# Kernel optimization log

Hardware: AMD Instinct MI355X
Metric: run time of the kernel (lower is better)

The kernel has to match this reference:

```python
import jax, jax.numpy as jnp
import numpy as np

B, H, W, C, HEADS = 32, 56, 56, 384, 12
WIN = (7, 7)
SHIFT = (3, 3)
N = WIN[0] * WIN[1]
HD = C // HEADS
HIDDEN = int(C * 2.0)
CPB_HIDDEN = 512


def _cpb_tables():
    # log-spaced continuous relative coordinates table (SwinV2 CPB)
    coords = [np.arange(-(w - 1), w, dtype=np.float32) for w in WIN]
    g = np.stack(np.meshgrid(*coords, indexing='ij'))
    for i, w in enumerate(WIN):
        g[i] = g[i] / (w - 1)
    rel = np.moveaxis(g, 0, -1)[None]              # (1, 2w0-1, 2w1-1, 2)
    rel = 8.0 * rel
    rel = np.sign(rel) * np.log2(np.abs(rel) + 1.0) / np.log2(8.0)
    grid = np.stack(np.meshgrid(*[np.arange(w) for w in WIN], indexing='ij')).reshape(2, -1)
    dists = grid[:, :, None] - grid[:, None, :]    # (2, N, N)
    dists[0] = (dists[0] + WIN[0] - 1) * (2 * WIN[1] - 1)
    dists[1] = (dists[1] + WIN[1] - 1)
    return jnp.asarray(rel, jnp.float32), jnp.asarray(dists.sum(0), jnp.int32)

REL_TAB, RPB_IDX = _cpb_tables()


def _compute_mask():
    img = np.zeros((1, H, W, 1), np.float32)
    cnt = 0
    for s0 in (slice(0, -WIN[0]), slice(-WIN[0], -SHIFT[0]), slice(-SHIFT[0], None)):
        for s1 in (slice(0, -WIN[1]), slice(-WIN[1], -SHIFT[1]), slice(-SHIFT[1], None)):
            img[:, s0, s1, :] = cnt
            cnt += 1
    w = img.reshape(1, H // WIN[0], WIN[0], W // WIN[1], WIN[1], 1)
    w = w.transpose(0, 1, 3, 2, 4, 5).reshape(-1, N)
    m = w[:, None, :] - w[:, :, None]
    return jnp.asarray(np.where(m != 0, -100.0, 0.0).astype(np.float32))


def _layernorm(x, g, b, eps=1e-5):
    mu = x.mean(-1, keepdims=True)
    var = ((x - mu) ** 2).mean(-1, keepdims=True)
    return (x - mu) / jnp.sqrt(var + eps) * g + b


def _window_partition(x):
    b = x.shape[0]
    x = x.reshape(b, H // WIN[0], WIN[0], W // WIN[1], WIN[1], C)
    return x.transpose(0, 1, 3, 2, 4, 5).reshape(-1, N, C)


def _window_reverse(win):
    x = win.reshape(B, H // WIN[0], W // WIN[1], WIN[0], WIN[1], C)
    return x.transpose(0, 1, 3, 2, 4, 5).reshape(B, H, W, C)


def setup_inputs() -> dict:
    key = jax.random.key(0)
    ks = jax.random.split(key, 16)
    s = 0.02
    return {
        'x': jax.random.normal(ks[0], (B, H, W, C), jnp.float32),
        'attn_mask': _compute_mask(),                              # (nW, N, N)
        'norm1_g': jnp.ones((C,), jnp.float32),
        'norm1_b': jnp.zeros((C,), jnp.float32),
        'qkv_w': jax.random.normal(ks[1], (3 * C, C), jnp.float32) * s,
        'qkv_b': jnp.zeros((3 * C,), jnp.float32),
        'proj_w': jax.random.normal(ks[2], (C, C), jnp.float32) * s,
        'proj_b': jnp.zeros((C,), jnp.float32),
        'cpb_w1': jax.random.normal(ks[3], (CPB_HIDDEN, 2), jnp.float32) * s,
        'cpb_b1': jnp.zeros((CPB_HIDDEN,), jnp.float32),
        'cpb_w2': jax.random.normal(ks[4], (HEADS, CPB_HIDDEN), jnp.float32) * s,
        'logit_scale': jnp.full((HEADS, 1, 1), np.log(10.0), jnp.float32),
        'norm2_g': jnp.ones((C,), jnp.float32),
        'norm2_b': jnp.zeros((C,), jnp.float32),
        'mlp_w1': jax.random.normal(ks[5], (HIDDEN, C), jnp.float32) * s,
        'mlp_b1': jnp.zeros((HIDDEN,), jnp.float32),
        'mlp_w2': jax.random.normal(ks[6], (C, HIDDEN), jnp.float32) * s,
        'mlp_b2': jnp.zeros((C,), jnp.float32),
    }


def reference(x, attn_mask, norm1_g, norm1_b, qkv_w, qkv_b, proj_w, proj_b,
              cpb_w1, cpb_b1, cpb_w2, logit_scale, norm2_g, norm2_b,
              mlp_w1, mlp_b1, mlp_w2, mlp_b2):
    # continuous position bias: MLP over log-spaced rel coords, gathered per pair
    h = jax.nn.relu(REL_TAB @ cpb_w1.T + cpb_b1)       # (1, 2w0-1, 2w1-1, 512)
    tab = (h @ cpb_w2.T).reshape(-1, HEADS)            # ((2w0-1)*(2w1-1), heads)
    rpb = tab[RPB_IDX.reshape(-1)].reshape(N, N, HEADS)
    rpb = 16.0 * jax.nn.sigmoid(rpb)
    rpb = rpb.transpose(2, 0, 1)                       # (heads, N, N)

    shortcut = x
    xn = _layernorm(x, norm1_g, norm1_b)
    xs = jnp.roll(xn, (-SHIFT[0], -SHIFT[1]), axis=(1, 2))
    wnd = _window_partition(xs)                        # (B*nW, N, C)
    qkv = (wnd @ qkv_w.T + qkv_b).reshape(-1, N, 3, HEADS, HD)
    q = qkv[:, :, 0].transpose(0, 2, 1, 3)             # (B*nW, heads, N, hd)
    k = qkv[:, :, 1].transpose(0, 2, 1, 3)
    v = qkv[:, :, 2].transpose(0, 2, 1, 3)
    qn = q / jnp.maximum(jnp.linalg.norm(q, axis=-1, keepdims=True), 1e-12)
    kn = k / jnp.maximum(jnp.linalg.norm(k, axis=-1, keepdims=True), 1e-12)
    scale = jnp.exp(jnp.minimum(logit_scale, jnp.log(100.0)))   # (heads,1,1)
    attn = jnp.einsum('bhnd,bhmd->bhnm', qn, kn) * scale + rpb
    nW = attn_mask.shape[0]
    attn = attn.reshape(B, nW, HEADS, N, N) + attn_mask[None, :, None]
    attn = jax.nn.softmax(attn.reshape(-1, HEADS, N, N), axis=-1)
    o = jnp.einsum('bhnm,bhmd->bhnd', attn, v)
    o = o.transpose(0, 2, 1, 3).reshape(-1, N, C)
    o = o @ proj_w.T + proj_b
    xr = _window_reverse(o)
    xr = jnp.roll(xr, (SHIFT[0], SHIFT[1]), axis=(1, 2))
    x = shortcut + xr
    xm = _layernorm(x, norm2_g, norm2_b)
    xm = jax.nn.gelu(xm @ mlp_w1.T + mlp_b1, approximate=False) @ mlp_w2.T + mlp_b2
    return x + xm
```

## Files before the change

### kernel.cpp

```cpp
#include <hip/hip_runtime.h>
#include <stdint.h>

typedef unsigned short u16;
typedef __bf16 bf16x8 __attribute__((ext_vector_type(8)));
typedef float f32x4 __attribute__((ext_vector_type(4)));

__device__ __forceinline__ float b2f(u16 u) {
    union { float f; uint32_t i; } x; x.i = ((uint32_t)u) << 16; return x.f;
}
__device__ __forceinline__ u16 f2b(float f) {
    union { float f; uint32_t i; } x; x.f = f;
    uint32_t r = (x.i + 0x7fffu + ((x.i >> 16) & 1u)) >> 16;
    return (u16)r;
}
__device__ __forceinline__ void gll16(const void* g, void* l) {
    __builtin_amdgcn_global_load_lds((const __attribute__((address_space(1))) void*)g,
                                     (__attribute__((address_space(3))) void*)l, 16, 0, 0);
}

__global__ __launch_bounds__(512)
void cpb_tab_kernel(const float* __restrict__ w1, const float* __restrict__ b1,
                    const float* __restrict__ w2, float* __restrict__ tab) {
    __shared__ float hbuf[512];
    int p = blockIdx.x, j = threadIdx.x;
    int i0 = p / 13, i1 = p % 13;
    float c0 = (i0 - 6) * (8.0f / 6.0f), c1 = (i1 - 6) * (8.0f / 6.0f);
    float r0 = copysignf(log2f(fabsf(c0) + 1.0f) * (1.0f / 3.0f), c0);
    float r1 = copysignf(log2f(fabsf(c1) + 1.0f) * (1.0f / 3.0f), c1);
    float h = r0 * w1[j * 2] + r1 * w1[j * 2 + 1] + b1[j];
    hbuf[j] = fmaxf(h, 0.0f);
    __syncthreads();
    if (j < 12) {
        float s = 0.0f;
        for (int t = 0; t < 512; t++) s += w2[j * 512 + t] * hbuf[t];
        tab[p * 12 + j] = s;
    }
}

__global__ __launch_bounds__(256)
void cpb_gather_kernel(const float* __restrict__ tab, float* __restrict__ rpb) {
    int idx = blockIdx.x * 256 + threadIdx.x;
    if (idx >= 12 * 2401) return;
    int h = idx / 2401, r = idx % 2401, i = r / 49, j = r % 49;
    int d = (i / 7 - j / 7 + 6) * 13 + (i % 7 - j % 7 + 6);
    float v = tab[d * 12 + h];
    rpb[idx] = 16.0f / (1.0f + expf(-v));
}

__global__ __launch_bounds__(256)
void wconv_kernel(const float* __restrict__ s0, const float* __restrict__ s1,
                  const float* __restrict__ s2, const float* __restrict__ s3,
                  u16* __restrict__ dst) {
    int i = (blockIdx.x * 256 + threadIdx.x) * 4;
    if (i >= 1179648) return;
    const float* src; int off;
    if (i < 442368)      { src = s0; off = i; }
    else if (i < 589824) { src = s1; off = i - 442368; }
    else if (i < 884736) { src = s2; off = i - 589824; }
    else                 { src = s3; off = i - 884736; }
    float4 v = *(const float4*)(src + off);
    u16 o[4] = {f2b(v.x), f2b(v.y), f2b(v.z), f2b(v.w)};
    *(uint2*)(dst + i) = *(const uint2*)o;
}

template <int PERM>
__global__ __launch_bounds__(256)
void ln_fused_kernel(const float* __restrict__ in, const float* __restrict__ g,
                     const float* __restrict__ b, u16* __restrict__ outb) {
    int wave = threadIdx.x >> 6, lane = threadIdx.x & 63;
    int tok = blockIdx.x * 4 + wave;
    size_t src = (size_t)tok * 384;
    float2 v[3];
    float s = 0.0f, s2 = 0.0f;
#pragma unroll
    for (int i = 0; i < 3; i++) {
        v[i] = *(const float2*)&in[src + i * 128 + lane * 2];
        s += v[i].x + v[i].y;
        s2 += v[i].x * v[i].x + v[i].y * v[i].y;
    }
#pragma unroll
    for (int m = 32; m >= 1; m >>= 1) { s += __shfl_xor(s, m, 64); s2 += __shfl_xor(s2, m, 64); }
    float mu = s * (1.0f / 384.0f);
    float rstd = rsqrtf(s2 * (1.0f / 384.0f) - mu * mu + 1e-5f);
    int drow = tok;
    if (PERM) {
        int bb = tok / 3136, rr = tok % 3136;
        int h = rr / 56, w = rr % 56;
        int hs = h - 3; if (hs < 0) hs += 56;
        int wsr = w - 3; if (wsr < 0) wsr += 56;
        int wi = (hs / 7) * 8 + (wsr / 7);
        int n = (hs % 7) * 7 + (wsr % 7);
        drow = (bb * 64 + wi) * 49 + n;
    }
    size_t dst = (size_t)drow * 384;
#pragma unroll
    for (int i = 0; i < 3; i++) {
        int c = i * 128 + lane * 2;
        float2 gg = *(const float2*)&g[c];
        float2 bv = *(const float2*)&b[c];
        u16 o[2] = { f2b((v[i].x - mu) * rstd * gg.x + bv.x),
                     f2b((v[i].y - mu) * rstd * gg.y + bv.y) };
        *(uint32_t*)&outb[dst + c] = *(const uint32_t*)o;
    }
}

enum { SRC_PLAIN = 0, SRC_HEADMAJ = 1 };
enum { EPI_QKV = 0, EPI_PROJ = 1, EPI_MLP1 = 2, EPI_MLP2 = 3 };

template <int SRC, int EPI, int GX>
__global__ __launch_bounds__(256)
void gemm_mfma(const u16* __restrict__ A, const u16* __restrict__ Wb,
               const float* __restrict__ bias, int K,
               u16* __restrict__ o0, u16* __restrict__ o1, u16* __restrict__ o2,
               const float* __restrict__ xres, float* __restrict__ dout) {
    const int tid = threadIdx.x;
    const int wave = tid >> 6, lane = tid & 63, quad = lane >> 4, l16 = lane & 15;
    const int wm = (wave >> 1) * 64, wn = (wave & 1) * 64;
    const int bid = blockIdx.x;
    const int nb = (bid & 7) * ((int)gridDim.x >> 3) + (bid >> 3);
    const int m0 = (nb / GX) * 128, n0 = (nb % GX) * 128;
    __shared__ alignas(16) u16 lA[128 * 32];
    __shared__ alignas(16) u16 lB[128 * 32];
    f32x4 acc[4][4] = {};

    const int c4 = lane & 3, rsub = lane >> 2;
    size_t agb[2], wgb[2];
#pragma unroll
    for (int s = 0; s < 2; s++) {
        int row = (wave * 2 + s) * 16 + rsub;
        int swz = (c4 ^ ((row >> 1) & 3)) * 16;
        int grow = m0 + row;
        if (SRC == SRC_HEADMAJ) {
            int widx = grow / 49, n = grow % 49;
            agb[s] = ((size_t)widx * 18816 + (size_t)n * 32) * 2 + swz;
        } else {
            agb[s] = (size_t)grow * (size_t)K * 2 + swz;
        }
        wgb[s] = (size_t)(n0 + row) * (size_t)K * 2 + swz;
    }
    const char* Ac = (const char*)A;
    const char* Wc = (const char*)Wb;
    char* ldsA = (char*)lA;
    char* ldsB = (char*)lB;
    const int swzR = (quad ^ ((l16 >> 1) & 3)) * 16;

    for (int kk = 0; kk < K; kk += 32) {
        __syncthreads();
        size_t ka = (SRC == SRC_HEADMAJ) ? (size_t)(kk >> 5) * 3136 : (size_t)kk * 2;
        size_t kb = (size_t)kk * 2;
#pragma unroll
        for (int s = 0; s < 2; s++)
            gll16(Ac + agb[s] + ka, ldsA + (wave * 2 + s) * 1024);
#pragma unroll
        for (int s = 0; s < 2; s++)
            gll16(Wc + wgb[s] + kb, ldsB + (wave * 2 + s) * 1024);
        __syncthreads();
        bf16x8 af[4], bfr[4];
#pragma unroll
        for (int t = 0; t < 4; t++)
            af[t] = *(const bf16x8*)(ldsA + (wm + t * 16 + l16) * 64 + swzR);
#pragma unroll
        for (int t = 0; t < 4; t++)
            bfr[t] = *(const bf16x8*)(ldsB + (wn + t * 16 + l16) * 64 + swzR);
#pragma unroll
        for (int i = 0; i < 4; i++)
#pragma unroll
            for (int j = 0; j < 4; j++)
                acc[i][j] = __builtin_amdgcn_mfma_f32_16x16x32_bf16(af[i], bfr[j], acc[i][j], 0, 0, 0);
    }

#pragma unroll
    for (int i = 0; i < 4; i++) {
#pragma unroll
        for (int r = 0; r < 4; r++) {
            int row = m0 + wm + i * 16 + quad * 4 + r;
            int widx = 0, n = 0;
            size_t pbase = 0;
            if (EPI == EPI_QKV || EPI == EPI_PROJ) { widx = row / 49; n = row % 49; }
            if (EPI == EPI_PROJ) {
                int bb = widx >> 6, wi = widx & 63;
                int hs = (wi >> 3) * 7 + n / 7, wsr = (wi & 7) * 7 + n % 7;
                int h = hs + 3; if (h >= 56) h -= 56;
                int w = wsr + 3; if (w >= 56) w -= 56;
                pbase = (((size_t)bb * 56 + h) * 56 + w) * 384;
            }
#pragma unroll
            for (int j = 0; j < 4; j++) {
                int col = n0 + wn + j * 16 + l16;
                float v = acc[i][j][r] + bias[col];
                if (EPI == EPI_QKV) {
                    int which = col / 384, head = (col >> 5) % 12, hd = col & 31;
                    u16* dst = (which == 0) ? o0 : ((which == 1) ? o1 : o2);
                    dst[(size_t)(widx * 12 + head) * 1568 + n * 32 + hd] = f2b(v);
                } else if (EPI == EPI_PROJ) {
                    dout[pbase + col] = v + xres[pbase + col];
                } else if (EPI == EPI_MLP1) {
                    float ge = 0.5f * v * (1.0f + erff(v * 0.70710678f));
                    o0[(size_t)row * 768 + col] = f2b(ge);
                } else {
                    size_t o = (size_t)row * 384 + col;
                    dout[o] = v + dout[o];
                }
            }
        }
    }
}

__global__ __launch_bounds__(256)
void attn_mfma_kernel(const u16* __restrict__ q, const u16* __restrict__ k,
                      const u16* __restrict__ v, const float* __restrict__ rpb,
                      const float* __restrict__ mask, const float* __restrict__ lsc,
                      u16* __restrict__ out) {
    __shared__ alignas(16) u16 sP[4][64 * 72];
    __shared__ alignas(16) u16 sVT[4][32 * 72];
    __shared__ float sQin[4][64], sKin[4][64];
    const int tid = threadIdx.x;
    const int wave = tid >> 6, lane = tid & 63;
    const int quad = lane >> 4, l16 = lane & 15;
    const int unit = blockIdx.x * 4 + wave;
    const int widx = unit / 12, head = unit - widx * 12;
    const size_t base = (size_t)unit * 1568;
    u16* pP  = sP[wave];
    u16* pVT = sVT[wave];
    float* qin = sQin[wave];
    float* kin = sKin[wave];

    if (lane >= 49) { qin[lane] = 0.0f; kin[lane] = 0.0f; }

    {
        const bool valid = lane < 49;
#pragma unroll
        for (int c = 0; c < 4; c++) {
            u16 r8[8] = {0, 0, 0, 0, 0, 0, 0, 0};
            if (valid) *(int4*)r8 = *(const int4*)&v[base + lane * 32 + c * 8];
#pragma unroll
            for (int e = 0; e < 8; e++) pVT[(c * 8 + e) * 72 + lane] = r8[e];
        }
    }

    const float lscale = __expf(fminf(lsc[head], 4.6051702f));
    bf16x8 qf[4], kf[4];
#pragma unroll
    for (int t = 0; t < 4; t++) {
        int row = t * 16 + l16; if (row > 48) row = 48;
        int4 qa = *(const int4*)&q[base + row * 32 + quad * 8];
        int4 ka = *(const int4*)&k[base + row * 32 + quad * 8];
        u16 qu[8], ku[8];
        *(int4*)qu = qa; *(int4*)ku = ka;
        float qs2 = 0.f, ks2 = 0.f;
#pragma unroll
        for (int e = 0; e < 8; e++) {
            float a = b2f(qu[e]), b = b2f(ku[e]);
            qs2 = fmaf(a, a, qs2); ks2 = fmaf(b, b, ks2);
        }
        qs2 += __shfl_xor(qs2, 16, 64); qs2 += __shfl_xor(qs2, 32, 64);
        ks2 += __shfl_xor(ks2, 16, 64); ks2 += __shfl_xor(ks2, 32, 64);
        if (quad == 0) {
            qin[row] = lscale * rsqrtf(fmaxf(qs2, 1e-24f));
            kin[row] = rsqrtf(fmaxf(ks2, 1e-24f));
        }
        qf[t] = *(bf16x8*)&qa;
        kf[t] = *(bf16x8*)&ka;
    }

    f32x4 s[4][4] = {};
#pragma unroll
    for (int mi = 0; mi < 4; mi++)
#pragma unroll
        for (int ni = 0; ni < 4; ni++)
            s[mi][ni] = __builtin_amdgcn_mfma_f32_16x16x32_bf16(qf[mi], kf[ni], s[mi][ni], 0, 0, 0);

    const float* rp = rpb + (size_t)head * 2401;
    const float* mk = mask + (size_t)(widx & 63) * 2401;
    float kj[4];
#pragma unroll
    for (int ni = 0; ni < 4; ni++) kj[ni] = kin[ni * 16 + l16];
#pragma unroll
    for (int mi = 0; mi < 4; mi++) {
#pragma unroll
        for (int r = 0; r < 4; r++) {
            const int i = mi * 16 + quad * 4 + r;
            const float qi = qin[i];
            const int ic = (i < 49 ? i : 48) * 49;
            const float* brow = rp + ic;
            const float* mrow = mk + ic;
            float lg[4];
#pragma unroll
            for (int ni = 0; ni < 4; ni++) {
                const int j = ni * 16 + l16;
                lg[ni] = (j < 49) ? fmaf(s[mi][ni][r], qi * kj[ni], brow[j] + mrow[j]) : -1e30f;
            }
            float m = fmaxf(fmaxf(lg[0], lg[1]), fmaxf(lg[2], lg[3]));
            m = fmaxf(m, __shfl_xor(m, 1, 64));
            m = fmaxf(m, __shfl_xor(m, 2, 64));
            m = fmaxf(m, __shfl_xor(m, 4, 64));
            m = fmaxf(m, __shfl_xor(m, 8, 64));
            float p0 = __expf(lg[0] - m), p1 = __expf(lg[1] - m);
            float p2 = __expf(lg[2] - m), p3 = __expf(lg[3] - m);
            float sum = p0 + p1 + p2 + p3;
            sum += __shfl_xor(sum, 1, 64);
            sum += __shfl_xor(sum, 2, 64);
            sum += __shfl_xor(sum, 4, 64);
            sum += __shfl_xor(sum, 8, 64);
            const float inv = 1.0f / sum;
            pP[i * 72 +  0 + l16] = f2b(p0 * inv);
            pP[i * 72 + 16 + l16] = f2b(p1 * inv);
            pP[i * 72 + 32 + l16] = f2b(p2 * inv);
            pP[i * 72 + 48 + l16] = f2b(p3 * inv);
        }
    }

    bf16x8 vf[2][2];
#pragma unroll
    for (int kk = 0; kk < 2; kk++)
#pragma unroll
        for (int ni = 0; ni < 2; ni++)
            vf[kk][ni] = *(const bf16x8*)&pVT[(ni * 16 + l16) * 72 + kk * 32 + quad * 8];
    f32x4 o[4][2] = {};
#pragma unroll
    for (int mi = 0; mi < 4; mi++)
#pragma unroll
        for (int kk = 0; kk < 2; kk++) {
            bf16x8 pa = *(const bf16x8*)&pP[(mi * 16 + l16) * 72 + kk * 32 + quad * 8];
#pragma unroll
            for (int ni = 0; ni < 2; ni++)
                o[mi][ni] = __builtin_amdgcn_mfma_f32_16x16x32_bf16(pa, vf[kk][ni], o[mi][ni], 0, 0, 0);
        }

#pragma unroll
    for (int mi = 0; mi < 4; mi++)
#pragma unroll
        for (int r = 0; r < 4; r++) {
            const int i = mi * 16 + quad * 4 + r;
            if (i < 49) {
                out[base + i * 32 + l16]      = f2b(o[mi][0][r]);
                out[base + i * 32 + 16 + l16] = f2b(o[mi][1][r]);
            }
        }
}

extern "C" void kernel_launch(void* const* d_in, const int* in_sizes, int n_in,
                              void* d_out, int out_size, void* d_ws, size_t ws_size,
                              hipStream_t stream) {
    const float* x      = (const float*)d_in[0];
    const float* mask   = (const float*)d_in[1];
    const float* n1g    = (const float*)d_in[2];
    const float* n1b    = (const float*)d_in[3];
    const float* qkv_w  = (const float*)d_in[4];
    const float* qkv_b  = (const float*)d_in[5];
    const float* proj_w = (const float*)d_in[6];
    const float* proj_b = (const float*)d_in[7];
    const float* cpb_w1 = (const float*)d_in[8];
    const float* cpb_b1 = (const float*)d_in[9];
    const float* cpb_w2 = (const float*)d_in[10];
    const float* lscale = (const float*)d_in[11];
    const float* n2g    = (const float*)d_in[12];
    const float* n2b    = (const float*)d_in[13];
    const float* mlp_w1 = (const float*)d_in[14];
    const float* mlp_b1 = (const float*)d_in[15];
    const float* mlp_w2 = (const float*)d_in[16];
    const float* mlp_b2 = (const float*)d_in[17];

    char* ws = (char*)d_ws;
    const size_t SLOT = 77070336ULL;
    float* tab = (float*)(ws);
    float* rpb = (float*)(ws + 16384);
    u16*  Wb   = (u16*)(ws + (1 << 20));
    u16*  qkv_wb  = Wb;
    u16*  proj_wb = Wb + 442368;
    u16*  mlp1_wb = Wb + 589824;
    u16*  mlp2_wb = Wb + 884736;
    u16* qb = (u16*)(ws + (4 << 20));
    u16* kb = (u16*)(ws + (4 << 20) + SLOT);
    u16* vb = (u16*)d_out;
    u16* xb = (u16*)((char*)d_out + SLOT);
    u16* attn_o = qb;
    u16* xb2    = kb;
    u16* hidden = qb;
    float* dout = (float*)d_out;

    wconv_kernel<<<1152, 256, 0, stream>>>(qkv_w, proj_w, mlp_w1, mlp_w2, Wb);
    cpb_tab_kernel<<<169, 512, 0, stream>>>(cpb_w1, cpb_b1, cpb_w2, tab);
    cpb_gather_kernel<<<113, 256, 0, stream>>>(tab, rpb);
    ln_fused_kernel<1><<<25088, 256, 0, stream>>>(x, n1g, n1b, xb);
    gemm_mfma<SRC_PLAIN, EPI_QKV, 9><<<7056, 256, 0, stream>>>(
        xb, qkv_wb, qkv_b, 384, qb, kb, vb, nullptr, nullptr);
    attn_mfma_kernel<<<6144, 256, 0, stream>>>(qb, kb, vb, rpb, mask, lscale, attn_o);
    gemm_mfma<SRC_HEADMAJ, EPI_PROJ, 3><<<2352, 256, 0, stream>>>(
        attn_o, proj_wb, proj_b, 384, nullptr, nullptr, nullptr, x, dout);
    ln_fused_kernel<0><<<25088, 256, 0, stream>>>(dout, n2g, n2b, xb2);
    for (int h = 0; h < 2; h++) {
        gemm_mfma<SRC_PLAIN, EPI_MLP1, 6><<<2352, 256, 0, stream>>>(
            xb2 + (size_t)h * 50176 * 384, mlp1_wb, mlp_b1, 384,
            hidden, nullptr, nullptr, nullptr, nullptr);
        gemm_mfma<SRC_PLAIN, EPI_MLP2, 3><<<1176, 256, 0, stream>>>(
            hidden, mlp2_wb, mlp_b2, 768, nullptr, nullptr, nullptr,
            nullptr, dout + (size_t)h * 50176 * 384);
    }
}
```

Before: 1.118 ms.

## Double-buffer GEMM LDS tiles with compile-time K and raise MFMA priority in attention

The GEMM's K loop now uses two LDS buffers. The global-to-LDS load for the next K step is issued before the MFMAs on the current step, so only one barrier is needed per step instead of two. K becomes a template parameter so the loop can be fully unrolled, and launch bounds now request 3 blocks per CU. The attention kernel wraps its two MFMA blocks in s_setprio so matrix work gets issue priority. In exchange, LDS use doubles to 32KB per block, and the unrolling plus occupancy hint may increase register pressure or cause spills.

```diff
diff --git a/kernel.cpp b/kernel.cpp
--- a/kernel.cpp
+++ b/kernel.cpp
@@ -107,10 +107,10 @@
 enum { SRC_PLAIN = 0, SRC_HEADMAJ = 1 };
 enum { EPI_QKV = 0, EPI_PROJ = 1, EPI_MLP1 = 2, EPI_MLP2 = 3 };
 
-template <int SRC, int EPI, int GX>
-__global__ __launch_bounds__(256)
+template <int SRC, int EPI, int GX, int K>
+__global__ __launch_bounds__(256, 3)
 void gemm_mfma(const u16* __restrict__ A, const u16* __restrict__ Wb,
-               const float* __restrict__ bias, int K,
+               const float* __restrict__ bias,
                u16* __restrict__ o0, u16* __restrict__ o1, u16* __restrict__ o2,
                const float* __restrict__ xres, float* __restrict__ dout) {
     const int tid = threadIdx.x;
@@ -119,8 +119,8 @@
     const int bid = blockIdx.x;
     const int nb = (bid & 7) * ((int)gridDim.x >> 3) + (bid >> 3);
     const int m0 = (nb / GX) * 128, n0 = (nb % GX) * 128;
-    __shared__ alignas(16) u16 lA[128 * 32];
-    __shared__ alignas(16) u16 lB[128 * 32];
+    __shared__ alignas(16) u16 lA[2][128 * 32];
+    __shared__ alignas(16) u16 lB[2][128 * 32];
     f32x4 acc[4][4] = {};
 
     const int c4 = lane & 3, rsub = lane >> 2;
@@ -140,34 +140,46 @@
     }
     const char* Ac = (const char*)A;
     const char* Wc = (const char*)Wb;
-    char* ldsA = (char*)lA;
-    char* ldsB = (char*)lB;
     const int swzR = (quad ^ ((l16 >> 1) & 3)) * 16;
-
-    for (int kk = 0; kk < K; kk += 32) {
-        __syncthreads();
-        size_t ka = (SRC == SRC_HEADMAJ) ? (size_t)(kk >> 5) * 3136 : (size_t)kk * 2;
-        size_t kb = (size_t)kk * 2;
-#pragma unroll
-        for (int s = 0; s < 2; s++)
-            gll16(Ac + agb[s] + ka, ldsA + (wave * 2 + s) * 1024);
-#pragma unroll
-        for (int s = 0; s < 2; s++)
-            gll16(Wc + wgb[s] + kb, ldsB + (wave * 2 + s) * 1024);
-        __syncthreads();
+    const int ldso = wave * 2048;
+
+#define STAGE(buf, step)                                                        \
+    {                                                                           \
+        size_t ka = (SRC == SRC_HEADMAJ) ? (size_t)(step) * 3136                \
+                                         : (size_t)(step) * 64;                 \
+        size_t kb = (size_t)(step) * 64;                                        \
+        char* la = (char*)lA[buf] + ldso;                                       \
+        char* lb = (char*)lB[buf] + ldso;                                       \
+        gll16(Ac + agb[0] + ka, la);                                            \
+        gll16(Ac + agb[1] + ka, la + 1024);                                     \
+        gll16(Wc + wgb[0] + kb, lb);                                            \
+        gll16(Wc + wgb[1] + kb, lb + 1024);                                     \
+    }
+
+    constexpr int NSTEP = K / 32;
+    STAGE(0, 0);
+    __syncthreads();
+#pragma unroll
+    for (int step = 0; step < NSTEP; step++) {
+        const int cur = step & 1;
+        if (step + 1 < NSTEP) STAGE(cur ^ 1, step + 1);
+        const char* la = (const char*)lA[cur];
+        const char* lb = (const char*)lB[cur];
         bf16x8 af[4], bfr[4];
 #pragma unroll
         for (int t = 0; t < 4; t++)
-            af[t] = *(const bf16x8*)(ldsA + (wm + t * 16 + l16) * 64 + swzR);
+            af[t] = *(const bf16x8*)(la + (wm + t * 16 + l16) * 64 + swzR);
 #pragma unroll
         for (int t = 0; t < 4; t++)
-            bfr[t] = *(const bf16x8*)(ldsB + (wn + t * 16 + l16) * 64 + swzR);
+            bfr[t] = *(const bf16x8*)(lb + (wn + t * 16 + l16) * 64 + swzR);
 #pragma unroll
         for (int i = 0; i < 4; i++)
 #pragma unroll
             for (int j = 0; j < 4; j++)
                 acc[i][j] = __builtin_amdgcn_mfma_f32_16x16x32_bf16(af[i], bfr[j], acc[i][j], 0, 0, 0);
-    }
+        if (step + 1 < NSTEP) __syncthreads();
+    }
+#undef STAGE
 
 #pragma unroll
     for (int i = 0; i < 4; i++) {
@@ -264,11 +276,13 @@
     }
 
     f32x4 s[4][4] = {};
+    __builtin_amdgcn_s_setprio(1);
 #pragma unroll
     for (int mi = 0; mi < 4; mi++)
 #pragma unroll
         for (int ni = 0; ni < 4; ni++)
             s[mi][ni] = __builtin_amdgcn_mfma_f32_16x16x32_bf16(qf[mi], kf[ni], s[mi][ni], 0, 0, 0);
+    __builtin_amdgcn_s_setprio(0);
 
     const float* rp = rpb + (size_t)head * 2401;
     const float* mk = mask + (size_t)(widx & 63) * 2401;
@@ -317,6 +331,7 @@
         for (int ni = 0; ni < 2; ni++)
             vf[kk][ni] = *(const bf16x8*)&pVT[(ni * 16 + l16) * 72 + kk * 32 + quad * 8];
     f32x4 o[4][2] = {};
+    __builtin_amdgcn_s_setprio(1);
 #pragma unroll
     for (int mi = 0; mi < 4; mi++)
 #pragma unroll
@@ -326,6 +341,7 @@
             for (int ni = 0; ni < 2; ni++)
                 o[mi][ni] = __builtin_amdgcn_mfma_f32_16x16x32_bf16(pa, vf[kk][ni], o[mi][ni], 0, 0, 0);
         }
+    __builtin_amdgcn_s_setprio(0);
 
 #pragma unroll
     for (int mi = 0; mi < 4; mi++)
@@ -383,18 +399,18 @@
     cpb_tab_kernel<<<169, 512, 0, stream>>>(cpb_w1, cpb_b1, cpb_w2, tab);
     cpb_gather_kernel<<<113, 256, 0, stream>>>(tab, rpb);
     ln_fused_kernel<1><<<25088, 256, 0, stream>>>(x, n1g, n1b, xb);
-    gemm_mfma<SRC_PLAIN, EPI_QKV, 9><<<7056, 256, 0, stream>>>(
-        xb, qkv_wb, qkv_b, 384, qb, kb, vb, nullptr, nullptr);
+    gemm_mfma<SRC_PLAIN, EPI_QKV, 9, 384><<<7056, 256, 0, stream>>>(
+        xb, qkv_wb, qkv_b, qb, kb, vb, nullptr, nullptr);
     attn_mfma_kernel<<<6144, 256, 0, stream>>>(qb, kb, vb, rpb, mask, lscale, attn_o);
-    gemm_mfma<SRC_HEADMAJ, EPI_PROJ, 3><<<2352, 256, 0, stream>>>(
-        attn_o, proj_wb, proj_b, 384, nullptr, nullptr, nullptr, x, dout);
+    gemm_mfma<SRC_HEADMAJ, EPI_PROJ, 3, 384><<<2352, 256, 0, stream>>>(
+        attn_o, proj_wb, proj_b, nullptr, nullptr, nullptr, x, dout);
     ln_fused_kernel<0><<<25088, 256, 0, stream>>>(dout, n2g, n2b, xb2);
     for (int h = 0; h < 2; h++) {
-        gemm_mfma<SRC_PLAIN, EPI_MLP1, 6><<<2352, 256, 0, stream>>>(
-            xb2 + (size_t)h * 50176 * 384, mlp1_wb, mlp_b1, 384,
+        gemm_mfma<SRC_PLAIN, EPI_MLP1, 6, 384><<<2352, 256, 0, stream>>>(
+            xb2 + (size_t)h * 50176 * 384, mlp1_wb, mlp_b1,
             hidden, nullptr, nullptr, nullptr, nullptr);
-        gemm_mfma<SRC_PLAIN, EPI_MLP2, 3><<<1176, 256, 0, stream>>>(
-            hidden, mlp2_wb, mlp_b2, 768, nullptr, nullptr, nullptr,
+        gemm_mfma<SRC_PLAIN, EPI_MLP2, 3, 768><<<1176, 256, 0, stream>>>(
+            hidden, mlp2_wb, mlp_b2, nullptr, nullptr, nullptr,
             nullptr, dout + (size_t)h * 50176 * 384);
     }
 }
```

Measured after the change: 1.079 ms. 3.5% less time.
